# Kernel optimization log

Measured on AMD Instinct MI355X. Metric: run time of the kernel, lower is better.

## Reference

```python
import jax, jax.numpy as jnp
import numpy as np

B, T, E, L, N, V = 512, 1005, 100, 10, 20, 32000


def prelu(x, a):
    return jnp.where(x >= 0, x, a * x)


def setup_inputs() -> dict:
    key = jax.random.key(0)
    ks = jax.random.split(key, 11)
    s = 0.1  # ~xavier std for 100x100
    return {
        "in_data": jax.random.normal(ks[0], (B, T, E), dtype=jnp.float32),
        "f": jax.random.normal(ks[1], (L, E), dtype=jnp.float32) * s,
        "h0": jax.random.normal(ks[2], (1, N, E), dtype=jnp.float32) * s,
        "w_mem": jax.random.normal(ks[3], (1, N, E), dtype=jnp.float32) * s,
        "U_w": jax.random.normal(ks[4], (E, E), dtype=jnp.float32) * s,
        "V_w": jax.random.normal(ks[5], (E, E), dtype=jnp.float32) * s,
        "W_w": jax.random.normal(ks[6], (E, E), dtype=jnp.float32) * s,
        "a_dm": jnp.full((1,), 0.25, dtype=jnp.float32),
        "H_w": jax.random.normal(ks[7], (E, E), dtype=jnp.float32) * s,
        "H_b": jax.random.normal(ks[8], (E,), dtype=jnp.float32) * s,
        "R_w": jax.random.normal(ks[9], (V, E), dtype=jnp.float32) * s,
        "R_b": jax.random.normal(ks[10], (V,), dtype=jnp.float32) * s,
        "a_out": jnp.full((1,), 0.25, dtype=jnp.float32),
    }


def reference(in_data, f, h0, w_mem, U_w, V_w, W_w, a_dm, H_w, H_b, R_w, R_b, a_out):
    n_full = T // L  # rest = T % L != 0 by construction -> torch loop runs n_full times
    rest = T % L
    # InputEncoder over all full sentences at once: [B, n_full, E]
    chunks = in_data[:, : n_full * L].reshape(B, n_full, L, E)
    infos = jnp.einsum("le,bnle->bne", f, chunks)
    # precompute V(w) term (constant across steps): [1, N, E]
    Vw = jnp.einsum("one,fe->onf", w_mem, V_w)

    def step(h, s):  # h: [B,N,E], s: [B,E]
        g = jax.nn.sigmoid(jnp.einsum("bne,be->bn", h + w_mem, s))[..., None]
        cand = prelu(
            jnp.einsum("bne,fe->bnf", h, U_w)
            + Vw
            + jnp.einsum("be,fe->bf", s, W_w)[:, None, :],
            a_dm,
        )
        h = h + g * cand
        h = h / jnp.linalg.norm(h, axis=2, keepdims=True)
        return h, None

    h_init = jnp.broadcast_to(h0, (B, N, E))
    h, _ = jax.lax.scan(step, h_init, jnp.swapaxes(infos, 0, 1))  # scan over sentences

    # query = InputEncoder on trailing remainder tokens
    q_tok = in_data[:, n_full * L :]  # [B, rest, E]
    q = jnp.einsum("le,ble->be", f[:rest], q_tok)  # [B, E]

    # OutputModule
    p = jax.nn.softmax(jnp.einsum("bne,be->bn", h, q), axis=1)  # [B, N]
    u = jnp.einsum("bn,bne->be", p, h)  # [B, E]
    y = q + u @ H_w.T + H_b
    return prelu(y, a_out) @ R_w.T + R_b  # [B, V]
```

## Files before the change

### kernel.cpp

```cpp
#include <hip/hip_runtime.h>
#include <hip/hip_bf16.h>

#define E      100
#define E2     112
#define NSLOT  20
#define BB     512
#define TT     1005
#define NFULL  100
#define LL     10
#define REST   5
#define VV     32000

typedef _Float16 f16x8 __attribute__((ext_vector_type(8)));
typedef _Float16 f16x4 __attribute__((ext_vector_type(4)));
typedef float    f32x16 __attribute__((ext_vector_type(16)));

__global__ __launch_bounds__(256) void k_cvt(
    const float* __restrict__ R_w, const float* __restrict__ W_w,
    const float* __restrict__ w_mem,
    _Float16* __restrict__ R16, _Float16* __restrict__ Wm16)
{
    const int gid = blockIdx.x * 256 + threadIdx.x;
    {
        int v = gid / 28, e4 = gid % 28;
        f16x4 o;
        if (e4 < 25) {
            float4 x = *(const float4*)&R_w[(size_t)v * E + e4 * 4];
            o[0] = (_Float16)x.x; o[1] = (_Float16)x.y;
            o[2] = (_Float16)x.z; o[3] = (_Float16)x.w;
        } else { o[0] = o[1] = o[2] = o[3] = (_Float16)0.f; }
        *(f16x4*)&R16[(size_t)v * E2 + e4 * 4] = o;
    }
    if (gid < 128 * 28) {
        int j = gid / 28, e4 = gid % 28;
        f16x4 o; o[0] = o[1] = o[2] = o[3] = (_Float16)0.f;
        if (e4 < 25 && j < 120) {
            float4 x = (j < 100) ? *(const float4*)&W_w[j * E + e4 * 4]
                                 : *(const float4*)&w_mem[(j - 100) * E + e4 * 4];
            o[0] = (_Float16)x.x; o[1] = (_Float16)x.y;
            o[2] = (_Float16)x.z; o[3] = (_Float16)x.w;
        }
        *(f16x4*)&Wm16[j * E2 + e4 * 4] = o;
    }
}

__global__ __launch_bounds__(256, 2) void k_prep(
    const float* __restrict__ in_data, const float* __restrict__ f,
    _Float16* __restrict__ s16, float* __restrict__ q_all)
{
    __shared__ float4 f4s[250];
    const int tid = threadIdx.x;
    const int b   = blockIdx.x;
    if (tid < 250) f4s[tid] = ((const float4*)f)[tid];
    __syncthreads();

    const size_t base = (size_t)b * TT * E;
    for (int idx = tid; idx < 2500; idx += 256) {
        int n = idx / 25, e4 = idx - n * 25;
        float4 a; a.x = a.y = a.z = a.w = 0.f;
        const float* xp = in_data + base + (size_t)(n * LL) * E + e4 * 4;
        #pragma unroll
        for (int l = 0; l < LL; ++l) {
            float4 x = *(const float4*)(xp + l * E);
            float4 fv = f4s[l * 25 + e4];
            a.x += fv.x * x.x; a.y += fv.y * x.y;
            a.z += fv.z * x.z; a.w += fv.w * x.w;
        }
        f16x4 o;
        o[0] = (_Float16)a.x; o[1] = (_Float16)a.y;
        o[2] = (_Float16)a.z; o[3] = (_Float16)a.w;
        *(f16x4*)&s16[((size_t)n * BB + b) * E2 + e4 * 4] = o;
    }
    for (int idx = tid; idx < 600; idx += 256) {
        int n = idx / 6, k = idx - n * 6;
        ((unsigned int*)s16)[(((size_t)n * BB + b) * E2 + 100) / 2 + k] = 0u;
    }
    if (tid < E) {
        const float* fp = (const float*)f4s;
        float a = 0.f;
        #pragma unroll
        for (int l = 0; l < REST; ++l)
            a += fp[l * E + tid] * in_data[base + (size_t)(NFULL * LL + l) * E + tid];
        q_all[(size_t)b * E + tid] = a;
    }
}

__global__ __launch_bounds__(256, 2) void k_mm(
    const _Float16* __restrict__ s16, const _Float16* __restrict__ Wm16,
    _Float16* __restrict__ sws16)
{
    __shared__ __align__(16) _Float16 AF[14 * 128 * 8];
    __shared__ __align__(16) _Float16 BF[14 * 128 * 8];
    const int tid  = threadIdx.x;
    const int mb   = blockIdx.x;
    const int lane = tid & 63;
    const int wv   = tid >> 6;
    const int half = lane >> 5;
    const int jt   = wv * 32 + (lane & 31);

    for (int idx = tid; idx < 128 * 14; idx += 256) {
        int m = idx / 14, c8 = idx - m * 14;
        *(f16x8*)&AF[(c8 * 128 + m) * 8] =
            *(const f16x8*)&s16[((size_t)mb * 128 + m) * E2 + c8 * 8];
        *(f16x8*)&BF[(c8 * 128 + m) * 8] =
            *(const f16x8*)&Wm16[m * E2 + c8 * 8];
    }
    __syncthreads();

    f16x8 Bfr[7];
    #pragma unroll
    for (int ck = 0; ck < 7; ++ck)
        Bfr[ck] = *(const f16x8*)&BF[((ck * 2 + half) * 128 + jt) * 8];

    #pragma unroll
    for (int Mt = 0; Mt < 4; ++Mt) {
        f32x16 acc;
        #pragma unroll
        for (int r = 0; r < 16; ++r) acc[r] = 0.f;
        #pragma unroll
        for (int ck = 0; ck < 7; ++ck) {
            f16x8 a = *(const f16x8*)&AF[((ck * 2 + half) * 128 + 32 * Mt + (lane & 31)) * 8];
            acc = __builtin_amdgcn_mfma_f32_32x32x16_f16(a, Bfr[ck], acc, 0, 0, 0);
        }
        #pragma unroll
        for (int r = 0; r < 16; ++r) {
            int row = 32 * Mt + (r & 3) + 8 * (r >> 2) + 4 * half;
            sws16[((size_t)mb * 128 + row) * 128 + jt] = (_Float16)acc[r];
        }
    }
}

#define BAR() do { asm volatile("s_waitcnt lgkmcnt(0)" ::: "memory"); \
                   __builtin_amdgcn_s_barrier(); } while (0)

__global__ __launch_bounds__(256, 2) void k_scan(
    const float* __restrict__ h0, const float* __restrict__ w_mem,
    const float* __restrict__ U_w, const float* __restrict__ V_w,
    const float* __restrict__ a_dm,
    const _Float16* __restrict__ s16, const _Float16* __restrict__ sws16,
    float* __restrict__ h_final)
{
    __shared__ __align__(16) _Float16 h16f[7 * 64 * 8];
    __shared__ __align__(16) _Float16 svL[2][128];
    __shared__ __align__(16) _Float16 swsL[2][128];
    __shared__ __align__(16) float    npL[32];
    __shared__ __align__(16) float    grawL[32];

    const int tid  = threadIdx.x;
    const int b    = blockIdx.x;
    const int lane = tid & 63;
    const int wv   = tid >> 6;
    const int col  = lane & 31;
    const int half = lane >> 5;
    const int fcol = wv * 32 + col;
    const int nval = half ? 8 : 12;
    const float adm = a_dm[0];

    f16x8 Bf[7];
    #pragma unroll
    for (int ck = 0; ck < 7; ++ck) {
        #pragma unroll
        for (int j = 0; j < 8; ++j) {
            int e = 16 * ck + 8 * half + j;
            Bf[ck][j] = (_Float16)((fcol < E && e < E) ? U_w[fcol * E + e] : 0.f);
        }
    }
    float VwC[16], hC[16];
    #pragma unroll
    for (int r = 0; r < 16; ++r) { VwC[r] = 0.f; hC[r] = 0.f; }
    for (int e4 = 0; e4 < 25; ++e4) {
        float4 v4 = make_float4(0.f, 0.f, 0.f, 0.f);
        if (fcol < E) v4 = *(const float4*)&V_w[fcol * E + e4 * 4];
        #pragma unroll
        for (int r = 0; r < 16; ++r) {
            if (r < nval) {
                int row = (r & 3) + 8 * (r >> 2) + 4 * half;
                float4 w4 = *(const float4*)&w_mem[row * E + e4 * 4];
                VwC[r] += w4.x * v4.x + w4.y * v4.y + w4.z * v4.z + w4.w * v4.w;
            }
        }
    }
    #pragma unroll
    for (int r = 0; r < 16; ++r) {
        if (r < nval) {
            int row = (r & 3) + 8 * (r >> 2) + 4 * half;
            if (fcol < E) hC[r] = h0[row * E + fcol];
        }
    }
    #pragma unroll
    for (int r = 0; r < 16; ++r) {
        int row = (r & 3) + 8 * (r >> 2) + 4 * half;
        if (fcol < E2) {
            int slot = (fcol >> 4) * 64 + ((fcol >> 3) & 1) * 32 + row;
            h16f[slot * 8 + (fcol & 7)] = (_Float16)((r < nval) ? hC[r] : 0.f);
        }
    }
    if (tid < E2) svL[0][tid] = s16[(size_t)b * E2 + tid];
    else if (tid >= 128) swsL[0][tid - 128] = sws16[(size_t)b * 128 + (tid - 128)];
    BAR();

    const unsigned short* s16u   = (const unsigned short*)s16;
    const unsigned short* sws16u = (const unsigned short*)sws16;

    for (int t = 0; t < NFULL; ++t) {
        const int p = t & 1;

        unsigned short nsv = 0, nsw = 0;
        if (t + 1 < NFULL) {
            if (tid < E2) nsv = s16u[((size_t)(t + 1) * BB + b) * E2 + tid];
            else if (tid >= 128) nsw = sws16u[((size_t)(t + 1) * BB + b) * 128 + (tid - 128)];
        }
        if (fcol == 100) {
            #pragma unroll
            for (int ck = 0; ck < 7; ++ck)
                Bf[ck] = *(const f16x8*)&svL[p][16 * ck + 8 * half];
        }
        f16x8 hA[7];
        #pragma unroll
        for (int ck = 0; ck < 7; ++ck)
            hA[ck] = *(const f16x8*)&h16f[(ck * 64 + lane) * 8];

        f32x16 acc;
        #pragma unroll
        for (int r = 0; r < 16; ++r) acc[r] = 0.f;
        #pragma unroll
        for (int ck = 0; ck < 7; ++ck)
            acc = __builtin_amdgcn_mfma_f32_32x32x16_f16(hA[ck], Bf[ck], acc, 0, 0, 0);

        if (wv == 0) {
            f32x16 acc2;
            #pragma unroll
            for (int r = 0; r < 16; ++r) acc2[r] = 0.f;
            #pragma unroll
            for (int ck = 0; ck < 7; ++ck)
                acc2 = __builtin_amdgcn_mfma_f32_32x32x16_f16(hA[ck], hA[ck], acc2, 0, 0, 0);
            #pragma unroll
            for (int r = 0; r < 16; ++r) {
                int row = (r & 3) + 8 * (r >> 2) + 4 * half;
                if (row < NSLOT && row == col) npL[row] = acc2[r];
            }
        }
        if (fcol == 100) {
            #pragma unroll
            for (int r = 0; r < 16; ++r) {
                int row = (r & 3) + 8 * (r >> 2) + 4 * half;
                if (row < NSLOT) grawL[row] = acc[r];
            }
        }
        BAR();

        const float swf = (fcol < E) ? (float)swsL[p][fcol] : 0.f;
        #pragma unroll
        for (int r = 0; r < 16; ++r) {
            if (r < nval) {
                int row = (r & 3) + 8 * (r >> 2) + 4 * half;
                float rn = (t == 0) ? 1.f : rsqrtf(npL[row]);
                float d  = fmaf(rn, grawL[row], (float)swsL[p][100 + row]);
                float g  = 1.f / (1.f + __expf(-d));
                float c  = fmaf(rn, acc[r], VwC[r] + swf);
                c = (c >= 0.f) ? c : adm * c;
                float hnew = fmaf(rn, hC[r], g * c);
                hC[r] = hnew;
                if (fcol < E) {
                    int slot = (fcol >> 4) * 64 + ((fcol >> 3) & 1) * 32 + row;
                    h16f[slot * 8 + (fcol & 7)] = (_Float16)hnew;
                }
            }
        }
        if (t + 1 < NFULL) {
            int pn = p ^ 1;
            if (tid < E2) ((unsigned short*)svL[pn])[tid] = nsv;
            else if (tid >= 128) ((unsigned short*)swsL[pn])[tid - 128] = nsw;
        }
        BAR();
    }

    {
        if (wv == 0) {
            f16x8 hA[7];
            #pragma unroll
            for (int ck = 0; ck < 7; ++ck)
                hA[ck] = *(const f16x8*)&h16f[(ck * 64 + lane) * 8];
            f32x16 acc2;
            #pragma unroll
            for (int r = 0; r < 16; ++r) acc2[r] = 0.f;
            #pragma unroll
            for (int ck = 0; ck < 7; ++ck)
                acc2 = __builtin_amdgcn_mfma_f32_32x32x16_f16(hA[ck], hA[ck], acc2, 0, 0, 0);
            #pragma unroll
            for (int r = 0; r < 16; ++r) {
                int row = (r & 3) + 8 * (r >> 2) + 4 * half;
                if (row < NSLOT && row == col) npL[row] = acc2[r];
            }
        }
        BAR();
        if (fcol < E) {
            #pragma unroll
            for (int r = 0; r < 16; ++r) {
                if (r < nval) {
                    int row = (r & 3) + 8 * (r >> 2) + 4 * half;
                    h_final[(size_t)b * NSLOT * E + row * E + fcol] = rsqrtf(npL[row]) * hC[r];
                }
            }
        }
    }
}

__global__ __launch_bounds__(256, 2) void k_attn(
    const float* __restrict__ h_final, const float* __restrict__ q_all,
    const float* __restrict__ H_w, const float* __restrict__ H_b,
    const float* __restrict__ a_out, _Float16* __restrict__ py16)
{
    __shared__ float Hl[E * 101];
    __shared__ float h_l[NSLOT * E];
    __shared__ float q_l[E], u_l[E];
    __shared__ float part[200], party[200];
    __shared__ float dl[NSLOT], pl[NSLOT];
    const int tid = threadIdx.x;
    const int b   = blockIdx.x;

    for (int idx = tid; idx < E * E; idx += 256) {
        int fr = idx / E, e = idx - fr * E;
        Hl[fr * 101 + e] = H_w[idx];
    }
    for (int idx = tid; idx < NSLOT * E; idx += 256)
        h_l[idx] = h_final[(size_t)b * NSLOT * E + idx];
    if (tid < E) q_l[tid] = q_all[(size_t)b * E + tid];
    __syncthreads();

    if (tid < 200) {
        int n = tid / 10, j = tid - n * 10;
        float a = 0.f;
        #pragma unroll
        for (int k = 0; k < 10; ++k) { int e = j * 10 + k; a += h_l[n * E + e] * q_l[e]; }
        part[tid] = a;
    }
    __syncthreads();
    if (tid < NSLOT) {
        float d = 0.f;
        #pragma unroll
        for (int j = 0; j < 10; ++j) d += part[tid * 10 + j];
        dl[tid] = d;
    }
    __syncthreads();
    if (tid < NSLOT) {
        float m = -1e30f;
        for (int i = 0; i < NSLOT; ++i) m = fmaxf(m, dl[i]);
        float s = 0.f;
        for (int i = 0; i < NSLOT; ++i) s += __expf(dl[i] - m);
        pl[tid] = __expf(dl[tid] - m) / s;
    }
    __syncthreads();
    if (tid < E) {
        float u = 0.f;
        for (int n = 0; n < NSLOT; ++n) u += pl[n] * h_l[n * E + tid];
        u_l[tid] = u;
    }
    __syncthreads();
    if (tid < 200) {
        int fr = tid % E, hf = tid / E;
        float a = 0.f;
        for (int e = hf * 50; e < hf * 50 + 50; ++e) a += u_l[e] * Hl[fr * 101 + e];
        party[tid] = a;
    }
    __syncthreads();
    if (tid < E2) {
        if (tid < E) {
            float y = q_l[tid] + H_b[tid] + party[tid] + party[100 + tid];
            const float ao = a_out[0];
            y = (y >= 0.f) ? y : ao * y;
            py16[(size_t)b * E2 + tid] = (_Float16)y;
        } else py16[(size_t)b * E2 + tid] = (_Float16)0.f;
    }
}

__global__ __launch_bounds__(256, 2) void k_out(
    const _Float16* __restrict__ py16, const _Float16* __restrict__ R16,
    const float* __restrict__ R_b, float* __restrict__ out)
{
    __shared__ __align__(16) _Float16 AF[14 * 128 * 8];
    __shared__ __align__(16) _Float16 BF[14 * 128 * 8];
    const int tid  = threadIdx.x;
    const int vb   = blockIdx.x;
    const int mb   = blockIdx.y;
    const int lane = tid & 63;
    const int wv   = tid >> 6;
    const int half = lane >> 5;
    const int jt   = wv * 32 + (lane & 31);
    const int v0   = vb * 128;

    for (int idx = tid; idx < 128 * 14; idx += 256) {
        int m = idx / 14, c8 = idx - m * 14;
        *(f16x8*)&AF[(c8 * 128 + m) * 8] =
            *(const f16x8*)&py16[((size_t)mb * 128 + m) * E2 + c8 * 8];
        *(f16x8*)&BF[(c8 * 128 + m) * 8] =
            *(const f16x8*)&R16[(size_t)(v0 + m) * E2 + c8 * 8];
    }
    __syncthreads();

    f16x8 Bfr[7];
    #pragma unroll
    for (int ck = 0; ck < 7; ++ck)
        Bfr[ck] = *(const f16x8*)&BF[((ck * 2 + half) * 128 + jt) * 8];
    const float rbv = R_b[v0 + jt];

    #pragma unroll
    for (int Mt = 0; Mt < 4; ++Mt) {
        f32x16 acc;
        #pragma unroll
        for (int r = 0; r < 16; ++r) acc[r] = 0.f;
        #pragma unroll
        for (int ck = 0; ck < 7; ++ck) {
            f16x8 a = *(const f16x8*)&AF[((ck * 2 + half) * 128 + 32 * Mt + (lane & 31)) * 8];
            acc = __builtin_amdgcn_mfma_f32_32x32x16_f16(a, Bfr[ck], acc, 0, 0, 0);
        }
        #pragma unroll
        for (int r = 0; r < 16; ++r) {
            int row = 32 * Mt + (r & 3) + 8 * (r >> 2) + 4 * half;
            out[((size_t)mb * 128 + row) * VV + v0 + jt] = acc[r] + rbv;
        }
    }
}

extern "C" void kernel_launch(void* const* d_in, const int* in_sizes, int n_in,
                              void* d_out, int out_size, void* d_ws, size_t ws_size,
                              hipStream_t stream)
{
    const float* in_data = (const float*)d_in[0];
    const float* f       = (const float*)d_in[1];
    const float* h0      = (const float*)d_in[2];
    const float* w_mem   = (const float*)d_in[3];
    const float* U_w     = (const float*)d_in[4];
    const float* V_w     = (const float*)d_in[5];
    const float* W_w     = (const float*)d_in[6];
    const float* a_dm    = (const float*)d_in[7];
    const float* H_w     = (const float*)d_in[8];
    const float* H_b     = (const float*)d_in[9];
    const float* R_w     = (const float*)d_in[10];
    const float* R_b     = (const float*)d_in[11];
    const float* a_out   = (const float*)d_in[12];
    float* out = (float*)d_out;

    char* ws = (char*)d_ws;
    _Float16* s16    = (_Float16*)(ws);
    _Float16* sws16  = (_Float16*)(ws + 11468800);
    _Float16* R16    = (_Float16*)(ws + 24576000);
    _Float16* Wm16   = (_Float16*)(ws + 31744000);
    float*    q_all  = (float*)   (ws + 31772672);
    float*    h_fin  = (float*)   (ws + 31977472);
    _Float16* py16   = (_Float16*)(ws + 36073472);

    k_cvt <<<3500, 256, 0, stream>>>(R_w, W_w, w_mem, R16, Wm16);
    k_prep<<<BB, 256, 0, stream>>>(in_data, f, s16, q_all);
    k_mm  <<<400, 256, 0, stream>>>(s16, Wm16, sws16);
    k_scan<<<BB, 256, 0, stream>>>(h0, w_mem, U_w, V_w, a_dm, s16, sws16, h_fin);
    k_attn<<<BB, 256, 0, stream>>>(h_fin, q_all, H_w, H_b, a_out, py16);
    k_out <<<dim3(VV / 128, 4), 256, 0, stream>>>(py16, R16, R_b, out);
}
```

Measured before the change: 651.7 us.

## Swizzle h16f LDS layout, compute gate once per slot and broadcast via bpermute

Changes the per-step LDS layout of the fp16 state matrix to an XOR-swizzled byte layout, so the scattered per-element writes and the vectorized MFMA operand loads hit fewer bank conflicts. The sigmoid gate and rsqrt norm are now computed once per slot lane and broadcast with ds_bpermute, replacing repeated LDS reads and transcendental work per accumulator row. Norm and gate values are packed into one float2 LDS array, register arrays shrink from 16 to 12, and fast rcp/rsq builtins are used. The norm MFMA moves from wave 0 to wave 1. This adds bpermute traffic and an initial zero-fill pass plus an extra barrier.

```diff
diff --git a/kernel.cpp b/kernel.cpp
--- a/kernel.cpp
+++ b/kernel.cpp
@@ -133,6 +133,12 @@
 #define BAR() do { asm volatile("s_waitcnt lgkmcnt(0)" ::: "memory"); \
                    __builtin_amdgcn_s_barrier(); } while (0)
 
+__device__ __forceinline__ f16x8 h_load(const _Float16* h16f, int ck, int lane) {
+    int byte = ck * 1024 + lane * 16;
+    byte ^= ((byte >> 9) & 3) << 5;
+    return *(const f16x8*)((const char*)h16f + byte);
+}
+
 __global__ __launch_bounds__(256, 2) void k_scan(
     const float* __restrict__ h0, const float* __restrict__ w_mem,
     const float* __restrict__ U_w, const float* __restrict__ V_w,
@@ -143,8 +149,7 @@
     __shared__ __align__(16) _Float16 h16f[7 * 64 * 8];
     __shared__ __align__(16) _Float16 svL[2][128];
     __shared__ __align__(16) _Float16 swsL[2][128];
-    __shared__ __align__(16) float    npL[32];
-    __shared__ __align__(16) float    grawL[32];
+    __shared__ __align__(16) float2   nggL[32];
 
     const int tid  = threadIdx.x;
     const int b    = blockIdx.x;
@@ -153,8 +158,10 @@
     const int col  = lane & 31;
     const int half = lane >> 5;
     const int fcol = wv * 32 + col;
-    const int nval = half ? 8 : 12;
     const float adm = a_dm[0];
+
+    const int hkey = ((fcol >> 3) & 3) << 5;
+    const int hbase = (fcol >> 3) * 512 + (fcol & 7) * 2 + 64 * half;
 
     f16x8 Bf[7];
     #pragma unroll
@@ -165,15 +172,15 @@
             Bf[ck][j] = (_Float16)((fcol < E && e < E) ? U_w[fcol * E + e] : 0.f);
         }
     }
-    float VwC[16], hC[16];
-    #pragma unroll
-    for (int r = 0; r < 16; ++r) { VwC[r] = 0.f; hC[r] = 0.f; }
+    float VwC[12], hC[12];
+    #pragma unroll
+    for (int r = 0; r < 12; ++r) { VwC[r] = 0.f; hC[r] = 0.f; }
     for (int e4 = 0; e4 < 25; ++e4) {
         float4 v4 = make_float4(0.f, 0.f, 0.f, 0.f);
         if (fcol < E) v4 = *(const float4*)&V_w[fcol * E + e4 * 4];
         #pragma unroll
-        for (int r = 0; r < 16; ++r) {
-            if (r < nval) {
+        for (int r = 0; r < 12; ++r) {
+            if (r < 8 || half == 0) {
                 int row = (r & 3) + 8 * (r >> 2) + 4 * half;
                 float4 w4 = *(const float4*)&w_mem[row * E + e4 * 4];
                 VwC[r] += w4.x * v4.x + w4.y * v4.y + w4.z * v4.z + w4.w * v4.w;
@@ -181,18 +188,23 @@
         }
     }
     #pragma unroll
-    for (int r = 0; r < 16; ++r) {
-        if (r < nval) {
+    for (int r = 0; r < 12; ++r) {
+        if (r < 8 || half == 0) {
             int row = (r & 3) + 8 * (r >> 2) + 4 * half;
             if (fcol < E) hC[r] = h0[row * E + fcol];
         }
     }
-    #pragma unroll
-    for (int r = 0; r < 16; ++r) {
-        int row = (r & 3) + 8 * (r >> 2) + 4 * half;
-        if (fcol < E2) {
-            int slot = (fcol >> 4) * 64 + ((fcol >> 3) & 1) * 32 + row;
-            h16f[slot * 8 + (fcol & 7)] = (_Float16)((r < nval) ? hC[r] : 0.f);
+    for (int idx = tid; idx < 896; idx += 256)
+        ((float2*)h16f)[idx] = make_float2(0.f, 0.f);
+    __syncthreads();
+    #pragma unroll
+    for (int r = 0; r < 12; ++r) {
+        if (r < 8 || half == 0) {
+            if (fcol < E) {
+                const int rc = (r & 3) + 8 * (r >> 2);
+                int byte = (hbase + rc * 16) ^ hkey;
+                *(_Float16*)((char*)h16f + byte) = (_Float16)hC[r];
+            }
         }
     }
     if (tid < E2) svL[0][tid] = s16[(size_t)b * E2 + tid];
@@ -218,7 +230,7 @@
         f16x8 hA[7];
         #pragma unroll
         for (int ck = 0; ck < 7; ++ck)
-            hA[ck] = *(const f16x8*)&h16f[(ck * 64 + lane) * 8];
+            hA[ck] = h_load(h16f, ck, lane);
 
         f32x16 acc;
         #pragma unroll
@@ -227,7 +239,7 @@
         for (int ck = 0; ck < 7; ++ck)
             acc = __builtin_amdgcn_mfma_f32_32x32x16_f16(hA[ck], Bf[ck], acc, 0, 0, 0);
 
-        if (wv == 0) {
+        if (wv == 1) {
             f32x16 acc2;
             #pragma unroll
             for (int r = 0; r < 16; ++r) acc2[r] = 0.f;
@@ -235,35 +247,45 @@
             for (int ck = 0; ck < 7; ++ck)
                 acc2 = __builtin_amdgcn_mfma_f32_32x32x16_f16(hA[ck], hA[ck], acc2, 0, 0, 0);
             #pragma unroll
-            for (int r = 0; r < 16; ++r) {
-                int row = (r & 3) + 8 * (r >> 2) + 4 * half;
-                if (row < NSLOT && row == col) npL[row] = acc2[r];
+            for (int r = 0; r < 12; ++r) {
+                if (r < 8 || half == 0) {
+                    int row = (r & 3) + 8 * (r >> 2) + 4 * half;
+                    if (row == col) nggL[row].x = acc2[r];
+                }
             }
         }
         if (fcol == 100) {
             #pragma unroll
-            for (int r = 0; r < 16; ++r) {
-                int row = (r & 3) + 8 * (r >> 2) + 4 * half;
-                if (row < NSLOT) grawL[row] = acc[r];
+            for (int r = 0; r < 12; ++r) {
+                if (r < 8 || half == 0) {
+                    int row = (r & 3) + 8 * (r >> 2) + 4 * half;
+                    nggL[row].y = acc[r];
+                }
             }
         }
         BAR();
 
         const float swf = (fcol < E) ? (float)swsL[p][fcol] : 0.f;
-        #pragma unroll
-        for (int r = 0; r < 16; ++r) {
-            if (r < nval) {
-                int row = (r & 3) + 8 * (r >> 2) + 4 * half;
-                float rn = (t == 0) ? 1.f : rsqrtf(npL[row]);
-                float d  = fmaf(rn, grawL[row], (float)swsL[p][100 + row]);
-                float g  = 1.f / (1.f + __expf(-d));
+        const int rw = (col < NSLOT) ? col : (NSLOT - 1);
+        float2 ng = nggL[rw];
+        float rn_l = (t == 0) ? 1.f : __builtin_amdgcn_rsqf(ng.x);
+        float d_l  = fmaf(rn_l, ng.y, (float)swsL[p][100 + rw]);
+        float g_l  = __builtin_amdgcn_rcpf(1.f + __expf(-d_l));
+
+        #pragma unroll
+        for (int r = 0; r < 12; ++r) {
+            if (r < 8 || half == 0) {
+                const int rc = (r & 3) + 8 * (r >> 2);
+                int bpi = rc * 4 + half * 16;
+                float rn = __int_as_float(__builtin_amdgcn_ds_bpermute(bpi, __float_as_int(rn_l)));
+                float g  = __int_as_float(__builtin_amdgcn_ds_bpermute(bpi, __float_as_int(g_l)));
                 float c  = fmaf(rn, acc[r], VwC[r] + swf);
                 c = (c >= 0.f) ? c : adm * c;
                 float hnew = fmaf(rn, hC[r], g * c);
                 hC[r] = hnew;
                 if (fcol < E) {
-                    int slot = (fcol >> 4) * 64 + ((fcol >> 3) & 1) * 32 + row;
-                    h16f[slot * 8 + (fcol & 7)] = (_Float16)hnew;
+                    int byte = (hbase + rc * 16) ^ hkey;
+                    *(_Float16*)((char*)h16f + byte) = (_Float16)hnew;
                 }
             }
         }
@@ -276,11 +298,11 @@
     }
 
     {
-        if (wv == 0) {
+        if (wv == 1) {
             f16x8 hA[7];
             #pragma unroll
             for (int ck = 0; ck < 7; ++ck)
-                hA[ck] = *(const f16x8*)&h16f[(ck * 64 + lane) * 8];
+                hA[ck] = h_load(h16f, ck, lane);
             f32x16 acc2;
             #pragma unroll
             for (int r = 0; r < 16; ++r) acc2[r] = 0.f;
@@ -288,18 +310,21 @@
             for (int ck = 0; ck < 7; ++ck)
                 acc2 = __builtin_amdgcn_mfma_f32_32x32x16_f16(hA[ck], hA[ck], acc2, 0, 0, 0);
             #pragma unroll
-            for (int r = 0; r < 16; ++r) {
-                int row = (r & 3) + 8 * (r >> 2) + 4 * half;
-                if (row < NSLOT && row == col) npL[row] = acc2[r];
+            for (int r = 0; r < 12; ++r) {
+                if (r < 8 || half == 0) {
+                    int row = (r & 3) + 8 * (r >> 2) + 4 * half;
+                    if (row == col) nggL[row].x = acc2[r];
+                }
             }
         }
         BAR();
         if (fcol < E) {
             #pragma unroll
-            for (int r = 0; r < 16; ++r) {
-                if (r < nval) {
+            for (int r = 0; r < 12; ++r) {
+                if (r < 8 || half == 0) {
                     int row = (r & 3) + 8 * (r >> 2) + 4 * half;
-                    h_final[(size_t)b * NSLOT * E + row * E + fcol] = rsqrtf(npL[row]) * hC[r];
+                    h_final[(size_t)b * NSLOT * E + row * E + fcol] =
+                        __builtin_amdgcn_rsqf(nggL[row].x) * hC[r];
                 }
             }
         }
```

After: 561.2 us. 1.16x faster.

## Transpose scan MFMA so slots map to columns, with swizzled LDS h layout

Applied to the files above, without the earlier changes.

Swaps the MFMA operand roles in the recurrent scan so U_w is the A operand and h is the B operand. Each lane now owns one memory slot (column) and 16 feature rows, which makes the per-slot norm and gate a single broadcast value per lane. The h buffer in LDS gets an XOR-swizzled layout written as packed f16x4 stores, and the norm and gate scalars are merged into one float2 array. It also uses the hardware rsq/rcp intrinsics and vectorized float4 output stores. The aim is fewer scalar LDS ops, fewer bank conflicts, and a cheaper elementwise update on the serial per-step critical path, at the cost of more complex indexing.

```diff
diff --git a/kernel.cpp b/kernel.cpp
--- a/kernel.cpp
+++ b/kernel.cpp
@@ -143,8 +143,7 @@
     __shared__ __align__(16) _Float16 h16f[7 * 64 * 8];
     __shared__ __align__(16) _Float16 svL[2][128];
     __shared__ __align__(16) _Float16 swsL[2][128];
-    __shared__ __align__(16) float    npL[32];
-    __shared__ __align__(16) float    grawL[32];
+    __shared__ __align__(16) float2   nggL[32];
 
     const int tid  = threadIdx.x;
     const int b    = blockIdx.x;
@@ -152,47 +151,65 @@
     const int wv   = tid >> 6;
     const int col  = lane & 31;
     const int half = lane >> 5;
-    const int fcol = wv * 32 + col;
-    const int nval = half ? 8 : 12;
     const float adm = a_dm[0];
 
-    f16x8 Bf[7];
+    int wb[4];
+    #pragma unroll
+    for (int q = 0; q < 4; ++q) {
+        int eq = 32 * wv + 4 * half + 8 * q;
+        int bp = (eq >> 3) * 512 + col * 16 + 8 * half;
+        wb[q] = bp ^ (((bp >> 9) & 3) << 5);
+    }
+    int rb[7];
+    #pragma unroll
+    for (int ck = 0; ck < 7; ++ck) {
+        int bp = ck * 1024 + lane * 16;
+        rb[ck] = bp ^ (((bp >> 9) & 3) << 5);
+    }
+
+    f16x8 Uf[7];
+    const int fA = 32 * wv + col;
     #pragma unroll
     for (int ck = 0; ck < 7; ++ck) {
         #pragma unroll
         for (int j = 0; j < 8; ++j) {
             int e = 16 * ck + 8 * half + j;
-            Bf[ck][j] = (_Float16)((fcol < E && e < E) ? U_w[fcol * E + e] : 0.f);
+            Uf[ck][j] = (_Float16)((fA < E && e < E) ? U_w[fA * E + e] : 0.f);
         }
     }
     float VwC[16], hC[16];
     #pragma unroll
     for (int r = 0; r < 16; ++r) { VwC[r] = 0.f; hC[r] = 0.f; }
     for (int e4 = 0; e4 < 25; ++e4) {
-        float4 v4 = make_float4(0.f, 0.f, 0.f, 0.f);
-        if (fcol < E) v4 = *(const float4*)&V_w[fcol * E + e4 * 4];
+        float4 w4 = make_float4(0.f, 0.f, 0.f, 0.f);
+        if (col < NSLOT) w4 = *(const float4*)&w_mem[col * E + e4 * 4];
         #pragma unroll
         for (int r = 0; r < 16; ++r) {
-            if (r < nval) {
-                int row = (r & 3) + 8 * (r >> 2) + 4 * half;
-                float4 w4 = *(const float4*)&w_mem[row * E + e4 * 4];
+            int f = 32 * wv + (r & 3) + 8 * (r >> 2) + 4 * half;
+            if (f < E) {
+                float4 v4 = *(const float4*)&V_w[f * E + e4 * 4];
                 VwC[r] += w4.x * v4.x + w4.y * v4.y + w4.z * v4.z + w4.w * v4.w;
             }
         }
     }
     #pragma unroll
     for (int r = 0; r < 16; ++r) {
-        if (r < nval) {
-            int row = (r & 3) + 8 * (r >> 2) + 4 * half;
-            if (fcol < E) hC[r] = h0[row * E + fcol];
-        }
-    }
-    #pragma unroll
-    for (int r = 0; r < 16; ++r) {
-        int row = (r & 3) + 8 * (r >> 2) + 4 * half;
-        if (fcol < E2) {
-            int slot = (fcol >> 4) * 64 + ((fcol >> 3) & 1) * 32 + row;
-            h16f[slot * 8 + (fcol & 7)] = (_Float16)((r < nval) ? hC[r] : 0.f);
+        int f = 32 * wv + (r & 3) + 8 * (r >> 2) + 4 * half;
+        if (col < NSLOT && f < E) hC[r] = h0[col * E + f];
+    }
+    for (int idx = tid; idx < 896; idx += 256)
+        ((float2*)h16f)[idx] = make_float2(0.f, 0.f);
+    __syncthreads();
+    if (col < NSLOT) {
+        #pragma unroll
+        for (int q = 0; q < 4; ++q) {
+            int f0 = 32 * wv + 4 * half + 8 * q;
+            if (f0 < E) {
+                f16x4 pk;
+                #pragma unroll
+                for (int i = 0; i < 4; ++i) pk[i] = (_Float16)hC[4 * q + i];
+                *(f16x4*)((char*)h16f + wb[q]) = pk;
+            }
         }
     }
     if (tid < E2) svL[0][tid] = s16[(size_t)b * E2 + tid];
@@ -210,60 +227,61 @@
             if (tid < E2) nsv = s16u[((size_t)(t + 1) * BB + b) * E2 + tid];
             else if (tid >= 128) nsw = sws16u[((size_t)(t + 1) * BB + b) * 128 + (tid - 128)];
         }
-        if (fcol == 100) {
+        if (wv == 3 && col == 4) {
             #pragma unroll
             for (int ck = 0; ck < 7; ++ck)
-                Bf[ck] = *(const f16x8*)&svL[p][16 * ck + 8 * half];
-        }
-        f16x8 hA[7];
+                Uf[ck] = *(const f16x8*)&svL[p][16 * ck + 8 * half];
+        }
+        f16x8 hB[7];
         #pragma unroll
         for (int ck = 0; ck < 7; ++ck)
-            hA[ck] = *(const f16x8*)&h16f[(ck * 64 + lane) * 8];
+            hB[ck] = *(const f16x8*)((const char*)h16f + rb[ck]);
 
         f32x16 acc;
         #pragma unroll
         for (int r = 0; r < 16; ++r) acc[r] = 0.f;
         #pragma unroll
         for (int ck = 0; ck < 7; ++ck)
-            acc = __builtin_amdgcn_mfma_f32_32x32x16_f16(hA[ck], Bf[ck], acc, 0, 0, 0);
-
-        if (wv == 0) {
+            acc = __builtin_amdgcn_mfma_f32_32x32x16_f16(Uf[ck], hB[ck], acc, 0, 0, 0);
+
+        if (wv == 1) {
             f32x16 acc2;
             #pragma unroll
             for (int r = 0; r < 16; ++r) acc2[r] = 0.f;
             #pragma unroll
             for (int ck = 0; ck < 7; ++ck)
-                acc2 = __builtin_amdgcn_mfma_f32_32x32x16_f16(hA[ck], hA[ck], acc2, 0, 0, 0);
+                acc2 = __builtin_amdgcn_mfma_f32_32x32x16_f16(hB[ck], hB[ck], acc2, 0, 0, 0);
             #pragma unroll
             for (int r = 0; r < 16; ++r) {
-                int row = (r & 3) + 8 * (r >> 2) + 4 * half;
-                if (row < NSLOT && row == col) npL[row] = acc2[r];
-            }
-        }
-        if (fcol == 100) {
-            #pragma unroll
-            for (int r = 0; r < 16; ++r) {
-                int row = (r & 3) + 8 * (r >> 2) + 4 * half;
-                if (row < NSLOT) grawL[row] = acc[r];
-            }
-        }
+                int rp = (r & 3) + 8 * (r >> 2) + 4 * half;
+                if (rp == col) nggL[col].x = acc2[r];
+            }
+        }
+        if (wv == 3 && half == 1) nggL[col].y = acc[0];
         BAR();
 
-        const float swf = (fcol < E) ? (float)swsL[p][fcol] : 0.f;
-        #pragma unroll
-        for (int r = 0; r < 16; ++r) {
-            if (r < nval) {
-                int row = (r & 3) + 8 * (r >> 2) + 4 * half;
-                float rn = (t == 0) ? 1.f : rsqrtf(npL[row]);
-                float d  = fmaf(rn, grawL[row], (float)swsL[p][100 + row]);
-                float g  = 1.f / (1.f + __expf(-d));
-                float c  = fmaf(rn, acc[r], VwC[r] + swf);
-                c = (c >= 0.f) ? c : adm * c;
-                float hnew = fmaf(rn, hC[r], g * c);
-                hC[r] = hnew;
-                if (fcol < E) {
-                    int slot = (fcol >> 4) * 64 + ((fcol >> 3) & 1) * 32 + row;
-                    h16f[slot * 8 + (fcol & 7)] = (_Float16)hnew;
+        float2 ng = nggL[col];
+        float rn = (t == 0) ? 1.f : __builtin_amdgcn_rsqf(ng.x);
+        float dd = fmaf(rn, ng.y, (float)swsL[p][100 + col]);
+        float g  = __builtin_amdgcn_rcpf(1.f + __expf(-dd));
+
+        if (col < NSLOT) {
+            #pragma unroll
+            for (int q = 0; q < 4; ++q) {
+                int f0 = 32 * wv + 4 * half + 8 * q;
+                if (f0 < E) {
+                    f16x4 sw4 = *(const f16x4*)&swsL[p][f0];
+                    f16x4 pk;
+                    #pragma unroll
+                    for (int i = 0; i < 4; ++i) {
+                        int r = 4 * q + i;
+                        float c = fmaf(rn, acc[r], VwC[r] + (float)sw4[i]);
+                        c = (c >= 0.f) ? c : adm * c;
+                        float hnew = fmaf(rn, hC[r], g * c);
+                        hC[r] = hnew;
+                        pk[i] = (_Float16)hnew;
+                    }
+                    *(f16x4*)((char*)h16f + wb[q]) = pk;
                 }
             }
         }
@@ -276,30 +294,36 @@
     }
 
     {
-        if (wv == 0) {
-            f16x8 hA[7];
+        if (wv == 1) {
+            f16x8 hB[7];
             #pragma unroll
             for (int ck = 0; ck < 7; ++ck)
-                hA[ck] = *(const f16x8*)&h16f[(ck * 64 + lane) * 8];
+                hB[ck] = *(const f16x8*)((const char*)h16f + rb[ck]);
             f32x16 acc2;
             #pragma unroll
             for (int r = 0; r < 16; ++r) acc2[r] = 0.f;
             #pragma unroll
             for (int ck = 0; ck < 7; ++ck)
-                acc2 = __builtin_amdgcn_mfma_f32_32x32x16_f16(hA[ck], hA[ck], acc2, 0, 0, 0);
+                acc2 = __builtin_amdgcn_mfma_f32_32x32x16_f16(hB[ck], hB[ck], acc2, 0, 0, 0);
             #pragma unroll
             for (int r = 0; r < 16; ++r) {
-                int row = (r & 3) + 8 * (r >> 2) + 4 * half;
-                if (row < NSLOT && row == col) npL[row] = acc2[r];
+                int rp = (r & 3) + 8 * (r >> 2) + 4 * half;
+                if (rp == col) nggL[col].x = acc2[r];
             }
         }
         BAR();
-        if (fcol < E) {
-            #pragma unroll
-            for (int r = 0; r < 16; ++r) {
-                if (r < nval) {
-                    int row = (r & 3) + 8 * (r >> 2) + 4 * half;
-                    h_final[(size_t)b * NSLOT * E + row * E + fcol] = rsqrtf(npL[row]) * hC[r];
+        float rn = __builtin_amdgcn_rsqf(nggL[col].x);
+        if (col < NSLOT) {
+            #pragma unroll
+            for (int q = 0; q < 4; ++q) {
+                int f0 = 32 * wv + 4 * half + 8 * q;
+                if (f0 < E) {
+                    float4 o;
+                    o.x = rn * hC[4 * q + 0];
+                    o.y = rn * hC[4 * q + 1];
+                    o.z = rn * hC[4 * q + 2];
+                    o.w = rn * hC[4 * q + 3];
+                    *(float4*)&h_final[(size_t)b * NSLOT * E + col * E + f0] = o;
                 }
             }
         }
```

After: 594.1 us. 1.1x faster.
